# Kernel optimization log

Hardware: AMD Instinct MI355X
Metric: run time of the kernel (lower is better)

## Reference

```python
import jax, jax.numpy as jnp
import numpy as np

EPS = 1e-8


def setup_inputs() -> dict:
    key = jax.random.key(0)
    k1, k2 = jax.random.split(key)
    a = jax.random.normal(k1, (1, 256, 128, 128), dtype=jnp.float32)
    b = jax.random.normal(k2, (1, 256, 128, 128), dtype=jnp.float32)
    return {"a": a, "b": b}


def reference(a, b):
    # a: [n, c, h, w] rendered feats; b: [n, c, h2, w2] style feats (n == 1)
    n, c, h, w = a.shape
    a_flat = a.reshape(n, c, -1)            # [n, c, hw]
    b_flat = b.reshape(n, c, -1)            # [n, c, h2w2]

    # argmin_cos_distance: channel-wise L2 normalize, cosine distance, argmin
    b_norm = jnp.sqrt((b_flat * b_flat).sum(1, keepdims=True) + EPS)
    b_n = b_flat / (b_norm + EPS)
    a_norm = jnp.sqrt((a_flat * a_flat).sum(1, keepdims=True) + EPS)
    a_n = a_flat / (a_norm + EPS)
    d_mat = 1.0 - jnp.einsum('ncp,ncq->npq', a_n, b_n)   # [n, hw, h2w2]
    z_best = jnp.argmin(d_mat, axis=2)                    # [n, hw]

    # nn_feat_replace: gather matched (unnormalized) style features
    idx = jnp.broadcast_to(z_best[:, None, :], b_flat.shape)
    target = jnp.take_along_axis(b_flat, idx, axis=2).reshape(n, c, h, w)

    # cos_loss(a, target): cosine distance over channel dim, mean over pixels
    an = jnp.sqrt((a * a).sum(1, keepdims=True))
    tn = jnp.sqrt((target * target).sum(1, keepdims=True))
    cossim = ((a / (an + EPS)) * (target / (tn + EPS))).sum(1)  # [n, h, w]
    return (1.0 - cossim).mean()
```

## Files before the change

kernel.cpp:

```cpp
#include <hip/hip_runtime.h>
#include <stdint.h>

#define EPS 1e-8f

constexpr int HW = 16384;
constexpr int BM = 128;
constexpr int NG = 2048;

typedef __attribute__((ext_vector_type(4))) float floatx4;
typedef __attribute__((ext_vector_type(4))) int   intx4;
typedef __attribute__((ext_vector_type(8))) int   intx8;
typedef unsigned char u8;
typedef unsigned int u32;
typedef unsigned long long u64;

typedef const __attribute__((address_space(1))) u32 gas_u32;
typedef __attribute__((address_space(3))) u32 las_u32;
__device__ inline void stage16(const void* g, void* l) {
    __builtin_amdgcn_global_load_lds((gas_u32*)g, (las_u32*)l, 16, 0, 0);
}

__device__ inline u32 pk4(float x0, float x1, float x2, float x3) {
    int t = __builtin_amdgcn_cvt_pk_fp8_f32(x0, x1, 0, false);
    t = __builtin_amdgcn_cvt_pk_fp8_f32(x2, x3, t, true);
    return (u32)t;
}

__global__ __launch_bounds__(512) void prep_kernel(const float* __restrict__ a,
                                                   const float* __restrict__ b,
                                                   float* __restrict__ sumsq_a,
                                                   float* __restrict__ sumsq_b,
                                                   u8* __restrict__ aF, u8* __restrict__ bF,
                                                   u64* __restrict__ packed,
                                                   float* __restrict__ out) {
    __shared__ float red[16][33];
    __shared__ float invb_sh[32];
    const int tid = threadIdx.x;
    const int px = tid & 31, cu = tid >> 5;
    const int p0 = blockIdx.x * 32;
    const int p = p0 + px;
    const int c0 = cu * 16;
    const u32 g = (u32)(p >> 4), r = (u32)(p & 15);
    const u32 sbase = g * 4096u + (u32)(cu >> 3) * 2048u + (u32)(cu & 1) * 1024u
                    + ((u32)((cu >> 1) & 3) * 16u + r) * 16u;

    if (blockIdx.x < 32) packed[(size_t)blockIdx.x * 512 + tid] = 0ull;
    if (blockIdx.x == 0 && tid == 0) *out = 0.f;

    float bv[16];
    float s = 0.f;
    #pragma unroll
    for (int e = 0; e < 16; ++e) {
        bv[e] = b[(size_t)(c0 + e) * HW + p];
        s += bv[e] * bv[e];
    }
    red[cu][px] = s;
    __syncthreads();
    if (tid < 32) {
        float B = 0.f;
        #pragma unroll
        for (int j = 0; j < 16; ++j) B += red[j][tid];
        sumsq_b[p0 + tid] = B;
        invb_sh[tid] = 1.0f / (sqrtf(B + EPS) + EPS);
    }
    __syncthreads();

    {
        const float inv = invb_sh[px];
        int4 W;
        W.x = (int)pk4(bv[0] * inv, bv[1] * inv, bv[2] * inv, bv[3] * inv);
        W.y = (int)pk4(bv[4] * inv, bv[5] * inv, bv[6] * inv, bv[7] * inv);
        W.z = (int)pk4(bv[8] * inv, bv[9] * inv, bv[10] * inv, bv[11] * inv);
        W.w = (int)pk4(bv[12] * inv, bv[13] * inv, bv[14] * inv, bv[15] * inv);
        *(int4*)(bF + sbase) = W;
    }

    {
        float av[16];
        s = 0.f;
        #pragma unroll
        for (int e = 0; e < 16; ++e) {
            av[e] = a[(size_t)(c0 + e) * HW + p];
            s += av[e] * av[e];
        }
        int4 W;
        W.x = (int)pk4(av[0], av[1], av[2], av[3]);
        W.y = (int)pk4(av[4], av[5], av[6], av[7]);
        W.z = (int)pk4(av[8], av[9], av[10], av[11]);
        W.w = (int)pk4(av[12], av[13], av[14], av[15]);
        *(int4*)(aF + sbase) = W;
    }
    red[cu][px] = s;
    __syncthreads();
    if (tid < 32) {
        float A = 0.f;
        #pragma unroll
        for (int j = 0; j < 16; ++j) A += red[j][tid];
        sumsq_a[p0 + tid] = A;
    }
}

#define MFMA1(A_, B_, C_) __builtin_amdgcn_mfma_scale_f32_16x16x128_f8f6f4( \
        (A_), (B_), (C_), 0, 0, 0, SCL, 0, SCL)

#define LDB(off_) __builtin_shufflevector(                                  \
        *(const intx4*)(Lb + (off_)), *(const intx4*)(Lb + (off_) + 1024),  \
        0, 1, 2, 3, 4, 5, 6, 7)

#define MFMA_QT(acc_, buf_) do {                                            \
    const u8* Lb = &sB[buf_][(u32)(wn * 2) * 4096u + (u32)lane * 16u];      \
    intx8 Bk0n0 = LDB(0);                                                   \
    intx8 Bk0n1 = LDB(4096);                                                \
    __builtin_amdgcn_s_setprio(1);                                          \
    _Pragma("unroll")                                                       \
    for (int mi = 0; mi < 4; ++mi) {                                        \
        acc_[mi][0] = MFMA1(Afr[mi][0], Bk0n0, C64);                        \
        acc_[mi][1] = MFMA1(Afr[mi][0], Bk0n1, C64);                        \
    }                                                                       \
    __builtin_amdgcn_s_setprio(0);                                          \
    intx8 Bk1n0 = LDB(2048);                                                \
    intx8 Bk1n1 = LDB(4096 + 2048);                                         \
    __builtin_amdgcn_s_setprio(1);                                          \
    _Pragma("unroll")                                                       \
    for (int mi = 0; mi < 4; ++mi) {                                        \
        acc_[mi][0] = MFMA1(Afr[mi][1], Bk1n0, acc_[mi][0]);                \
        acc_[mi][1] = MFMA1(Afr[mi][1], Bk1n1, acc_[mi][1]);                \
    }                                                                       \
    __builtin_amdgcn_s_setprio(0);                                          \
} while (0)

#define ARGMAX_QT(acc_, qt_) do {                                           \
    const u32 qb_ = qbase + (u32)(qt_) * 64u;                               \
    _Pragma("unroll")                                                       \
    for (int mi = 0; mi < 4; ++mi) {                                        \
        _Pragma("unroll")                                                   \
        for (int ni = 0; ni < 2; ++ni) {                                    \
            const u32 qc_ = qb_ + (u32)(ni * 16);                           \
            _Pragma("unroll")                                               \
            for (int rr = 0; rr < 4; ++rr) {                                \
                float v_ = acc_[mi][ni][rr];                                \
                bool gt_ = v_ > bestv[mi][rr];                              \
                bestv[mi][rr] = gt_ ? v_ : bestv[mi][rr];                   \
                bestq[mi][rr] = gt_ ? qc_ : bestq[mi][rr];                  \
            }                                                               \
        }                                                                   \
    }                                                                       \
} while (0)

#define STAGE(buf_, qt_) do {                                               \
    const u8* gs_ = gQ + (u32)(qt_) * 16384u + so;                          \
    u8* ls_ = &sB[buf_][w * 4096];                                          \
    stage16(gs_,        ls_);                                               \
    stage16(gs_ + 1024, ls_ + 1024);                                        \
    stage16(gs_ + 2048, ls_ + 2048);                                        \
    stage16(gs_ + 3072, ls_ + 3072);                                        \
} while (0)

__global__ __launch_bounds__(256, 2) void gemm_argmax(const u8* __restrict__ aF,
                                                      const u8* __restrict__ bF,
                                                      u64* __restrict__ packed) {
    __shared__ u8 sB[2][16384];
    const int tid = threadIdx.x;
    const int w = tid >> 6, lane = tid & 63;
    const int q4 = lane >> 4, r15 = lane & 15;
    const int wm = w >> 1, wn = w & 1;

    const u32 bid = blockIdx.x;
    const u32 ng = bid & 7;
    const u32 mt = bid >> 3;
    const int p0 = (int)mt * BM;

    const u8* gA = aF + (((size_t)(mt * 8 + wm * 4)) << 12) + (u32)lane * 16;
    intx8 Afr[4][2];
    #pragma unroll
    for (int mi = 0; mi < 4; ++mi)
        #pragma unroll
        for (int kb = 0; kb < 2; ++kb)
            Afr[mi][kb] = __builtin_shufflevector(
                *(const intx4*)(gA + (u32)(mi * 4096 + kb * 2048)),
                *(const intx4*)(gA + (u32)(mi * 4096 + kb * 2048 + 1024)),
                0, 1, 2, 3, 4, 5, 6, 7);

    const u8* gQ = bF + ((size_t)ng << 19);
    const u32 so = (u32)w * 4096u + (u32)lane * 16u;

    float bestv[4][4];
    u32   bestq[4][4];
    #pragma unroll
    for (int mi = 0; mi < 4; ++mi)
        #pragma unroll
        for (int rr = 0; rr < 4; ++rr) { bestv[mi][rr] = -3.4e38f; bestq[mi][rr] = 0; }

    const u32 qbase = ng * 2048 + wn * 32 + (u32)r15;
    const floatx4 C64 = {64.f, 64.f, 64.f, 64.f};
    const int SCL = 0x7F7F7F7F;

    floatx4 accA[4][2], accB[4][2];

    STAGE(0, 0);
    __syncthreads();

    STAGE(1, 1);
    MFMA_QT(accA, 0);
    __syncthreads();

    for (int e = 0; e < 32; e += 2) {
        const int o = e + 1;
        if (o + 1 < 32) STAGE(0, o + 1);
        MFMA_QT(accB, 1);
        ARGMAX_QT(accA, e);
        __syncthreads();

        if (o + 1 < 32) {
            STAGE(1, o + 2);
            MFMA_QT(accA, 0);
            ARGMAX_QT(accB, o);
            __syncthreads();
        } else {
            ARGMAX_QT(accB, o);
        }
    }

    #pragma unroll
    for (int mi = 0; mi < 4; ++mi)
        #pragma unroll
        for (int rr = 0; rr < 4; ++rr) {
            u64 pk = ((u64)__float_as_uint(bestv[mi][rr]) << 32)
                   | (u64)(0xFFFFFFFFu - bestq[mi][rr]);
            #pragma unroll
            for (int d = 1; d < 16; d <<= 1) {
                u64 oV = __shfl_xor((unsigned long long)pk, d);
                pk = oV > pk ? oV : pk;
            }
            if (r15 == 0)
                atomicMax(&packed[p0 + wm * 64 + mi * 16 + q4 * 4 + rr], pk);
        }
}

__global__ void loss_kernel(const u64* __restrict__ packed,
                            const float* __restrict__ sumsq_a, const float* __restrict__ sumsq_b,
                            float* __restrict__ out) {
    int p = blockIdx.x * 256 + threadIdx.x;
    u64 pk = packed[p];
    float s = __uint_as_float((u32)(pk >> 32)) - 64.0f;
    u32 q = 0xFFFFFFFFu - (u32)(pk & 0xFFFFFFFFull);
    float A = sumsq_a[p], B = sumsq_b[q];
    float dot = s * (sqrtf(B + EPS) + EPS);
    float cossim = dot / ((sqrtf(A) + EPS) * (sqrtf(B) + EPS));
    float v = (1.0f - cossim) * (1.0f / (float)HW);
    #pragma unroll
    for (int d = 1; d < 64; d <<= 1) v += __shfl_xor(v, d);
    if ((threadIdx.x & 63) == 0) atomicAdd(out, v);
}

extern "C" void kernel_launch(void* const* d_in, const int* in_sizes, int n_in,
                              void* d_out, int out_size, void* d_ws, size_t ws_size,
                              hipStream_t stream) {
    const float* a = (const float*)d_in[0];
    const float* b = (const float*)d_in[1];
    float* out = (float*)d_out;
    char* ws = (char*)d_ws;

    u8*    aF      = (u8*)ws;
    u8*    bF      = (u8*)(ws + (size_t)4 * 1024 * 1024);
    float* sumsq_a = (float*)(ws + (size_t)8 * 1024 * 1024);
    float* sumsq_b = sumsq_a + HW;
    u64*   packed  = (u64*)(sumsq_b + HW);

    prep_kernel<<<dim3(HW / 32), 512, 0, stream>>>(a, b, sumsq_a, sumsq_b, aF, bF, packed, out);
    gemm_argmax<<<dim3((HW / BM) * (HW / NG)), 256, 0, stream>>>(aF, bF, packed);
    loss_kernel<<<dim3(HW / 256), 256, 0, stream>>>(packed, sumsq_a, sumsq_b, out);
}
```

Baseline: 147.8 us.

## Triple-buffer B tiles with one barrier per tile and vmcnt waits

Moves from a double-buffered LDS ring with two __syncthreads per iteration pair to a three-slot ring. Each tile now needs only one s_barrier, guarded by an explicit s_waitcnt vmcnt(4) so the next tile's global-to-LDS copy can stay in flight. MFMA and argmax now run on a single accumulator per tile instead of ping-ponging two accumulator sets, which lowers register pressure. LDS use rises to 48KB per block, which could limit the two-blocks-per-CU occupancy, and correctness depends on the hand-written vmcnt accounting.

```diff
diff --git a/kernel.cpp b/kernel.cpp
--- a/kernel.cpp
+++ b/kernel.cpp
@@ -107,15 +107,26 @@
         *(const intx4*)(Lb + (off_)), *(const intx4*)(Lb + (off_) + 1024),  \
         0, 1, 2, 3, 4, 5, 6, 7)
 
-#define MFMA_QT(acc_, buf_) do {                                            \
-    const u8* Lb = &sB[buf_][(u32)(wn * 2) * 4096u + (u32)lane * 16u];      \
+#define STAGE(slot_, qt_) do {                                              \
+    const u8* gs_ = gQ + (u32)(qt_) * 16384u + so;                          \
+    u8* ls_ = sB0 + (u32)(slot_) * 16384u + wso;                            \
+    stage16(gs_,        ls_);                                               \
+    stage16(gs_ + 1024, ls_ + 1024);                                        \
+    stage16(gs_ + 2048, ls_ + 2048);                                        \
+    stage16(gs_ + 3072, ls_ + 3072);                                        \
+} while (0)
+
+#define COMPUTE_QT(sc_, qc_) do {                                           \
+    const u8* Lb = sB0 + (u32)(sc_) * 16384u                                \
+                 + (u32)(wn * 2) * 4096u + (u32)lane * 16u;                 \
+    floatx4 acc[4][2];                                                      \
     intx8 Bk0n0 = LDB(0);                                                   \
     intx8 Bk0n1 = LDB(4096);                                                \
     __builtin_amdgcn_s_setprio(1);                                          \
     _Pragma("unroll")                                                       \
     for (int mi = 0; mi < 4; ++mi) {                                        \
-        acc_[mi][0] = MFMA1(Afr[mi][0], Bk0n0, C64);                        \
-        acc_[mi][1] = MFMA1(Afr[mi][0], Bk0n1, C64);                        \
+        acc[mi][0] = MFMA1(Afr[mi][0], Bk0n0, C64);                         \
+        acc[mi][1] = MFMA1(Afr[mi][0], Bk0n1, C64);                         \
     }                                                                       \
     __builtin_amdgcn_s_setprio(0);                                          \
     intx8 Bk1n0 = LDB(2048);                                                \
@@ -123,43 +134,31 @@
     __builtin_amdgcn_s_setprio(1);                                          \
     _Pragma("unroll")                                                       \
     for (int mi = 0; mi < 4; ++mi) {                                        \
-        acc_[mi][0] = MFMA1(Afr[mi][1], Bk1n0, acc_[mi][0]);                \
-        acc_[mi][1] = MFMA1(Afr[mi][1], Bk1n1, acc_[mi][1]);                \
+        acc[mi][0] = MFMA1(Afr[mi][1], Bk1n0, acc[mi][0]);                  \
+        acc[mi][1] = MFMA1(Afr[mi][1], Bk1n1, acc[mi][1]);                  \
     }                                                                       \
     __builtin_amdgcn_s_setprio(0);                                          \
-} while (0)
-
-#define ARGMAX_QT(acc_, qt_) do {                                           \
-    const u32 qb_ = qbase + (u32)(qt_) * 64u;                               \
     _Pragma("unroll")                                                       \
     for (int mi = 0; mi < 4; ++mi) {                                        \
         _Pragma("unroll")                                                   \
         for (int ni = 0; ni < 2; ++ni) {                                    \
-            const u32 qc_ = qb_ + (u32)(ni * 16);                           \
+            const u32 qn_ = (qc_) + (u32)(ni * 16);                         \
             _Pragma("unroll")                                               \
             for (int rr = 0; rr < 4; ++rr) {                                \
-                float v_ = acc_[mi][ni][rr];                                \
+                float v_ = acc[mi][ni][rr];                                 \
                 bool gt_ = v_ > bestv[mi][rr];                              \
                 bestv[mi][rr] = gt_ ? v_ : bestv[mi][rr];                   \
-                bestq[mi][rr] = gt_ ? qc_ : bestq[mi][rr];                  \
+                bestq[mi][rr] = gt_ ? qn_ : bestq[mi][rr];                  \
             }                                                               \
         }                                                                   \
     }                                                                       \
 } while (0)
 
-#define STAGE(buf_, qt_) do {                                               \
-    const u8* gs_ = gQ + (u32)(qt_) * 16384u + so;                          \
-    u8* ls_ = &sB[buf_][w * 4096];                                          \
-    stage16(gs_,        ls_);                                               \
-    stage16(gs_ + 1024, ls_ + 1024);                                        \
-    stage16(gs_ + 2048, ls_ + 2048);                                        \
-    stage16(gs_ + 3072, ls_ + 3072);                                        \
-} while (0)
-
 __global__ __launch_bounds__(256, 2) void gemm_argmax(const u8* __restrict__ aF,
                                                       const u8* __restrict__ bF,
                                                       u64* __restrict__ packed) {
-    __shared__ u8 sB[2][16384];
+    __shared__ u8 sB[3][16384];
+    u8* sB0 = &sB[0][0];
     const int tid = threadIdx.x;
     const int w = tid >> 6, lane = tid & 63;
     const int q4 = lane >> 4, r15 = lane & 15;
@@ -182,7 +181,8 @@
                 0, 1, 2, 3, 4, 5, 6, 7);
 
     const u8* gQ = bF + ((size_t)ng << 19);
-    const u32 so = (u32)w * 4096u + (u32)lane * 16u;
+    const u32 so  = (u32)w * 4096u + (u32)lane * 16u;
+    const u32 wso = (u32)w * 4096u;
 
     float bestv[4][4];
     u32   bestq[4][4];
@@ -191,35 +191,30 @@
         #pragma unroll
         for (int rr = 0; rr < 4; ++rr) { bestv[mi][rr] = -3.4e38f; bestq[mi][rr] = 0; }
 
-    const u32 qbase = ng * 2048 + wn * 32 + (u32)r15;
+    u32 qcur = ng * 2048 + wn * 32 + (u32)r15;
     const floatx4 C64 = {64.f, 64.f, 64.f, 64.f};
     const int SCL = 0x7F7F7F7F;
 
-    floatx4 accA[4][2], accB[4][2];
-
     STAGE(0, 0);
-    __syncthreads();
-
     STAGE(1, 1);
-    MFMA_QT(accA, 0);
-    __syncthreads();
-
-    for (int e = 0; e < 32; e += 2) {
-        const int o = e + 1;
-        if (o + 1 < 32) STAGE(0, o + 1);
-        MFMA_QT(accB, 1);
-        ARGMAX_QT(accA, e);
-        __syncthreads();
-
-        if (o + 1 < 32) {
-            STAGE(1, o + 2);
-            MFMA_QT(accA, 0);
-            ARGMAX_QT(accB, o);
-            __syncthreads();
-        } else {
-            ARGMAX_QT(accB, o);
+
+    int sc = 0;
+    for (int t = 0; t < 31; ++t) {
+        asm volatile("s_waitcnt vmcnt(4)" ::: "memory");
+        __builtin_amdgcn_sched_barrier(0);
+        __builtin_amdgcn_s_barrier();
+        if (t < 30) {
+            const int s2 = sc == 0 ? 2 : sc - 1;
+            STAGE(s2, t + 2);
         }
-    }
+        COMPUTE_QT(sc, qcur);
+        qcur += 64u;
+        sc = sc == 2 ? 0 : sc + 1;
+    }
+    asm volatile("s_waitcnt vmcnt(0)" ::: "memory");
+    __builtin_amdgcn_sched_barrier(0);
+    __builtin_amdgcn_s_barrier();
+    COMPUTE_QT(sc, qcur);
 
     #pragma unroll
     for (int mi = 0; mi < 4; ++mi)
```

Result: faster. 140.0 us (-5.3%).
